# Optimization experiments

Measured on AMD Instinct MI355X. Metric: run time of the kernel, lower is better.

Reference implementation:

```python
import jax, jax.numpy as jnp
import numpy as np

EPS = 1e-8
INTRA_MARGIN_USED = 1.5  # combine() swaps margins: intra gets delta_dist
INTER_MARGIN_USED = 0.5  # inter gets delta_var
INTRA_W, INTER_W, REG_W = 1.0, 1.0, 0.001


def setup_inputs() -> dict:
    key = jax.random.key(0)
    k1, k2 = jax.random.split(key)
    N, D, K = 1000000, 32, 64
    features = jax.random.normal(k1, (N, D), dtype=jnp.float32)
    labels = jax.random.randint(k2, (N,), 0, K, dtype=jnp.int64 if jax.config.jax_enable_x64 else jnp.int32)
    return {"features": features, "labels": labels, "num_clusters": K}


def reference(features, labels, num_clusters):
    K = int(num_clusters)
    N, D = features.shape
    ones = jnp.ones((N,), dtype=features.dtype)
    counts = jax.ops.segment_sum(ones, labels, num_segments=K)            # (K,)
    sums = jax.ops.segment_sum(features, labels, num_segments=K)          # (K, D)
    safe_counts = jnp.maximum(counts, 1.0)
    means = sums / safe_counts[:, None]                                   # (K, D) cluster centroids

    # --- intra (variance) loss; margin = 1.5 due to original swap ---
    diff = features - means[labels] + EPS                                 # (N, D)
    dists = jnp.sqrt(jnp.sum(diff * diff, axis=1))                        # (N,)
    hinge2 = jnp.square(jnp.maximum(dists - INTRA_MARGIN_USED, 0.0))
    per_cluster = jax.ops.segment_sum(hinge2, labels, num_segments=K) / safe_counts
    intra_loss = jnp.mean(per_cluster)

    # --- inter (distance) loss; margin = 0.5 due to original swap ---
    pdiff = means[:, None, :] - means[None, :, :] + EPS                   # (K, K, D)
    pdist = jnp.sqrt(jnp.sum(pdiff * pdiff, axis=-1))                     # (K, K)
    hinge = jnp.square(jnp.maximum(2.0 * INTER_MARGIN_USED - pdist, 0.0))
    offdiag = 1.0 - jnp.eye(K, dtype=features.dtype)
    inter_loss = jnp.sum(hinge * offdiag) / float((K - 1) * K)

    # --- regularization ---
    reg_loss = jnp.mean(jnp.sqrt(jnp.sum(jnp.square(means + EPS), axis=1)))

    total = INTRA_W * intra_loss + INTER_W * inter_loss + REG_W * reg_loss
    return total
```

## Files before the change

### kernel.cpp

```cpp
#include <hip/hip_runtime.h>
#include <math.h>


#define EPS_F 1e-8f
constexpr int D = 32;
constexpr int K = 64;
constexpr int NPTS = 1024;
constexpr int P1 = K * D + K;
constexpr int NCH = 64;
constexpr int NBLK2 = 2048;
constexpr int MPAD = 40;

__global__ __launch_bounds__(256, 4) void pass1_kernel(
    const float* __restrict__ feat, const int* __restrict__ lab,
    float* __restrict__ part1, float* __restrict__ sums, int N)
{
    __shared__ int            s_lab[NPTS];
    __shared__ unsigned short s_idx[NPTS];
    __shared__ int            s_hist[K];
    __shared__ int            s_pref[K];
    __shared__ int            s_cur[K];

    const int tid = threadIdx.x;
    const long long base = (long long)blockIdx.x * NPTS;
    int npts = (int)((long long)N - base);
    if (npts > NPTS) npts = NPTS;

    if (blockIdx.x == 0)
        for (int e = tid; e < P1; e += 256) sums[e] = 0.f;

    if (tid < K) s_hist[tid] = 0;
    __syncthreads();

    const int n4 = npts >> 2;
    for (int i4 = tid; i4 < n4; i4 += 256) {
        const int4 v = ((const int4*)(lab + base))[i4];
        s_lab[i4 * 4 + 0] = v.x; s_lab[i4 * 4 + 1] = v.y;
        s_lab[i4 * 4 + 2] = v.z; s_lab[i4 * 4 + 3] = v.w;
        atomicAdd(&s_hist[v.x], 1); atomicAdd(&s_hist[v.y], 1);
        atomicAdd(&s_hist[v.z], 1); atomicAdd(&s_hist[v.w], 1);
    }
    for (int i = (n4 << 2) + tid; i < npts; i += 256) {
        const int l = lab[base + i];
        s_lab[i] = l;
        atomicAdd(&s_hist[l], 1);
    }
    __syncthreads();

    if (tid < 64) {
        const int h = s_hist[tid];
        int v = h;
        for (int off = 1; off < 64; off <<= 1) {
            const int up = __shfl_up(v, off);
            if (tid >= off) v += up;
        }
        s_pref[tid] = v - h;
        s_cur[tid]  = v - h;
    }
    __syncthreads();

    for (int i = tid; i < npts; i += 256) {
        const int l = s_lab[i];
        const int pos = atomicAdd(&s_cur[l], 1);
        s_idx[pos] = (unsigned short)i;
    }
    __syncthreads();

    const int k = tid >> 2, q = tid & 3;
    const int start = s_pref[k], len = s_hist[k];
    float4 a0 = {0.f, 0.f, 0.f, 0.f}, a1 = {0.f, 0.f, 0.f, 0.f};
    int i = 0;
    for (; i + 4 <= len; i += 4) {
        const int i0 = s_idx[start + i + 0];
        const int i1 = s_idx[start + i + 1];
        const int i2 = s_idx[start + i + 2];
        const int i3 = s_idx[start + i + 3];
        const float4* r0 = (const float4*)(feat + (base + i0) * D + q * 8);
        const float4* r1 = (const float4*)(feat + (base + i1) * D + q * 8);
        const float4* r2 = (const float4*)(feat + (base + i2) * D + q * 8);
        const float4* r3 = (const float4*)(feat + (base + i3) * D + q * 8);
        const float4 x0 = r0[0], y0 = r0[1];
        const float4 x1 = r1[0], y1 = r1[1];
        const float4 x2 = r2[0], y2 = r2[1];
        const float4 x3 = r3[0], y3 = r3[1];
        a0.x += (x0.x + x1.x) + (x2.x + x3.x);
        a0.y += (x0.y + x1.y) + (x2.y + x3.y);
        a0.z += (x0.z + x1.z) + (x2.z + x3.z);
        a0.w += (x0.w + x1.w) + (x2.w + x3.w);
        a1.x += (y0.x + y1.x) + (y2.x + y3.x);
        a1.y += (y0.y + y1.y) + (y2.y + y3.y);
        a1.z += (y0.z + y1.z) + (y2.z + y3.z);
        a1.w += (y0.w + y1.w) + (y2.w + y3.w);
    }
    for (; i < len; ++i) {
        const int i0 = s_idx[start + i];
        const float4* r0 = (const float4*)(feat + (base + i0) * D + q * 8);
        const float4 x0 = r0[0], y0 = r0[1];
        a0.x += x0.x; a0.y += x0.y; a0.z += x0.z; a0.w += x0.w;
        a1.x += y0.x; a1.y += y0.y; a1.z += y0.z; a1.w += y0.w;
    }
    float* outp = part1 + (long long)blockIdx.x * P1;
    ((float4*)outp)[tid * 2 + 0] = a0;
    ((float4*)outp)[tid * 2 + 1] = a1;
    if (tid < K) outp[K * D + tid] = (float)s_hist[tid];
}

__global__ __launch_bounds__(256) void reduce1_kernel(
    const float* __restrict__ part1, float* __restrict__ sums,
    int chsz, int nblk1)
{
    const int e = blockIdx.x * 256 + threadIdx.x;
    if (e >= P1) return;
    const int y = blockIdx.y;
    const int b0 = y * chsz;
    int b1 = b0 + chsz; if (b1 > nblk1) b1 = nblk1;
    float s = 0.f;
    for (int b = b0; b < b1; b++) s += part1[(long long)b * P1 + e];
    atomicAdd(&sums[e], s);
}

__global__ __launch_bounds__(256, 4) void pass2_kernel(
    const float* __restrict__ feat, const int* __restrict__ lab,
    const float* __restrict__ sums,
    float* __restrict__ hpart, float* __restrict__ ir, int N)
{
    __shared__ float s_m[K * MPAD];
    __shared__ float s_ic[K];
    __shared__ float s_red[256];
    const int tid = threadIdx.x;

    for (int e = tid; e < K * D; e += 256) {
        const float c = sums[K * D + (e >> 5)];
        s_m[(e >> 5) * MPAD + (e & 31)] = sums[e] / fmaxf(c, 1.0f);
    }
    if (tid < K) s_ic[tid] = 1.0f / fmaxf(sums[K * D + tid], 1.0f);
    __syncthreads();

    float racc = 0.f;
    const long long stride = (long long)NBLK2 * 256;
    for (long long p = (long long)blockIdx.x * 256 + tid; p < N; p += stride) {
        const int l = lab[p];
        const float4* frow = (const float4*)(feat + p * D);
        float4 fv[8];
        #pragma unroll
        for (int j = 0; j < 8; j++) fv[j] = frow[j];
        const float* mrow = s_m + l * MPAD;
        float d2 = 0.f;
        #pragma unroll
        for (int j = 0; j < 8; j++) {
            const float4 mv = *(const float4*)(mrow + j * 4);
            const float dx = fv[j].x - mv.x + EPS_F;
            const float dy = fv[j].y - mv.y + EPS_F;
            const float dz = fv[j].z - mv.z + EPS_F;
            const float dw = fv[j].w - mv.w + EPS_F;
            d2 += dx * dx + dy * dy + dz * dz + dw * dw;
        }
        const float h = fmaxf(sqrtf(d2) - 1.5f, 0.f);
        racc += h * h * s_ic[l];
    }
    s_red[tid] = racc;
    __syncthreads();
    for (int st = 128; st; st >>= 1) { if (tid < st) s_red[tid] += s_red[tid + st]; __syncthreads(); }
    if (tid == 0) hpart[blockIdx.x] = s_red[0];

    if (blockIdx.x != 0) return;
    __syncthreads();
    float mj[32];
    const int j = tid & 63;
    #pragma unroll
    for (int d = 0; d < 32; d++) mj[d] = s_m[j * MPAD + d];
    float isum = 0.f;
    const int igrp = tid >> 6;
    for (int ii = 0; ii < 16; ii++) {
        const int i = igrp * 16 + ii;
        const float4* srow = (const float4*)(s_m + i * MPAD);
        float d2 = 0.f;
        #pragma unroll
        for (int q = 0; q < 8; q++) {
            const float4 mv = srow[q];
            const float b0 = mv.x - mj[q * 4 + 0] + EPS_F;
            const float b1 = mv.y - mj[q * 4 + 1] + EPS_F;
            const float b2 = mv.z - mj[q * 4 + 2] + EPS_F;
            const float b3 = mv.w - mj[q * 4 + 3] + EPS_F;
            d2 += b0 * b0 + b1 * b1 + b2 * b2 + b3 * b3;
        }
        if (i != j) {
            const float h = fmaxf(1.0f - sqrtf(d2), 0.f);
            isum += h * h;
        }
    }
    s_red[tid] = isum;
    __syncthreads();
    for (int st = 128; st; st >>= 1) { if (tid < st) s_red[tid] += s_red[tid + st]; __syncthreads(); }
    if (tid == 0) ir[0] = s_red[0] * (1.0f / ((K - 1) * K));
    __syncthreads();

    float r = 0.f;
    if (tid < 64) {
        float d2 = 0.f;
        #pragma unroll
        for (int d = 0; d < 32; d++) { const float t = mj[d] + EPS_F; d2 += t * t; }
        r = sqrtf(d2);
    }
    s_red[tid] = r;
    __syncthreads();
    for (int st = 128; st; st >>= 1) { if (tid < st) s_red[tid] += s_red[tid + st]; __syncthreads(); }
    if (tid == 0) ir[1] = s_red[0] * (1.0f / K);
}

__global__ __launch_bounds__(256) void final_kernel(
    const float* __restrict__ hpart, const float* __restrict__ ir,
    float* __restrict__ out)
{
    __shared__ float s_red[256];
    const int tid = threadIdx.x;
    float hs = 0.f;
    for (int b = tid; b < NBLK2; b += 256) hs += hpart[b];
    s_red[tid] = hs;
    __syncthreads();
    for (int st = 128; st; st >>= 1) { if (tid < st) s_red[tid] += s_red[tid + st]; __syncthreads(); }
    if (tid == 0) out[0] = s_red[0] * (1.0f / K) + ir[0] + 0.001f * ir[1];
}

extern "C" void kernel_launch(void* const* d_in, const int* in_sizes, int n_in,
                              void* d_out, int out_size, void* d_ws, size_t ws_size,
                              hipStream_t stream)
{
    const float* feat = (const float*)d_in[0];
    const int*   lab  = (const int*)d_in[1];
    const int N = in_sizes[1];

    float* ws = (float*)d_ws;

    const int nblk1 = (N + NPTS - 1) / NPTS;
    const int chsz  = (nblk1 + NCH - 1) / NCH;

    float* sums  = ws;
    float* ir    = sums + P1;
    float* hpart = ir + 4;
    float* part1 = hpart + NBLK2;

    pass1_kernel<<<nblk1, 256, 0, stream>>>(feat, lab, part1, sums, N);
    reduce1_kernel<<<dim3((P1 + 255) / 256, NCH), 256, 0, stream>>>(part1, sums, chsz, nblk1);
    pass2_kernel<<<NBLK2, 256, 0, stream>>>(feat, lab, sums, hpart, ir, N);
    final_kernel<<<1, 256, 0, stream>>>(hpart, ir, (float*)d_out);
}
```

Baseline: 61.99 us.

## Stage feature tiles in LDS for coalesced per-cluster sums in pass1

The first pass now loads each block's feature tile with contiguous float4 loads into a padded shared-memory tile. The per-cluster gather-and-sum then reads from LDS instead of issuing scattered global loads by sorted index. Labels are read one per thread, the tile shrinks to 512 points, and blocks grow to 512 threads, each thread summing one float4 column slice per cluster. The aim is to replace uncoalesced global gathers with coalesced streaming. The cost is large LDS use per block, which limits occupancy, and twice as many partial rows for the reduction kernel to read.

```diff
diff --git a/kernel.cpp b/kernel.cpp
--- a/kernel.cpp
+++ b/kernel.cpp
@@ -5,46 +5,52 @@
 #define EPS_F 1e-8f
 constexpr int D = 32;
 constexpr int K = 64;
-constexpr int NPTS = 1024;
+constexpr int NPTS = 512;
+constexpr int RSTRIDE = 36;
 constexpr int P1 = K * D + K;
 constexpr int NCH = 64;
 constexpr int NBLK2 = 2048;
 constexpr int MPAD = 40;
 
-__global__ __launch_bounds__(256, 4) void pass1_kernel(
+constexpr int L_TILE = NPTS * RSTRIDE;
+constexpr int L_IDX  = L_TILE;
+constexpr int L_HIST = L_IDX + NPTS / 2;
+constexpr int L_PREF = L_HIST + K;
+constexpr int L_CUR  = L_PREF + K;
+constexpr int L_TOTAL = L_CUR + K;
+
+__global__ __launch_bounds__(512) void pass1_kernel(
     const float* __restrict__ feat, const int* __restrict__ lab,
     float* __restrict__ part1, float* __restrict__ sums, int N)
 {
-    __shared__ int            s_lab[NPTS];
-    __shared__ unsigned short s_idx[NPTS];
-    __shared__ int            s_hist[K];
-    __shared__ int            s_pref[K];
-    __shared__ int            s_cur[K];
+    extern __shared__ float smem[];
+    float*          s_tile = smem;
+    unsigned short* s_idx  = (unsigned short*)(smem + L_IDX);
+    int*            s_hist = (int*)(smem + L_HIST);
+    int*            s_pref = (int*)(smem + L_PREF);
+    int*            s_cur  = (int*)(smem + L_CUR);
 
     const int tid = threadIdx.x;
     const long long base = (long long)blockIdx.x * NPTS;
     int npts = (int)((long long)N - base);
     if (npts > NPTS) npts = NPTS;
+    const int nf4 = npts * 8;
 
     if (blockIdx.x == 0)
-        for (int e = tid; e < P1; e += 256) sums[e] = 0.f;
+        for (int e = tid; e < P1; e += 512) sums[e] = 0.f;
+
+    const int myl = (tid < npts) ? lab[base + tid] : -1;
+    float4 st[8];
+    const float4* fsrc = (const float4*)(feat + base * D);
+    #pragma unroll
+    for (int u = 0; u < 8; u++) {
+        const int g = tid + u * 512;
+        if (g < nf4) st[u] = fsrc[g];
+    }
 
     if (tid < K) s_hist[tid] = 0;
     __syncthreads();
-
-    const int n4 = npts >> 2;
-    for (int i4 = tid; i4 < n4; i4 += 256) {
-        const int4 v = ((const int4*)(lab + base))[i4];
-        s_lab[i4 * 4 + 0] = v.x; s_lab[i4 * 4 + 1] = v.y;
-        s_lab[i4 * 4 + 2] = v.z; s_lab[i4 * 4 + 3] = v.w;
-        atomicAdd(&s_hist[v.x], 1); atomicAdd(&s_hist[v.y], 1);
-        atomicAdd(&s_hist[v.z], 1); atomicAdd(&s_hist[v.w], 1);
-    }
-    for (int i = (n4 << 2) + tid; i < npts; i += 256) {
-        const int l = lab[base + i];
-        s_lab[i] = l;
-        atomicAdd(&s_hist[l], 1);
-    }
+    if (myl >= 0) atomicAdd(&s_hist[myl], 1);
     __syncthreads();
 
     if (tid < 64) {
@@ -59,49 +65,44 @@
     }
     __syncthreads();
 
-    for (int i = tid; i < npts; i += 256) {
-        const int l = s_lab[i];
-        const int pos = atomicAdd(&s_cur[l], 1);
-        s_idx[pos] = (unsigned short)i;
-    }
-    __syncthreads();
-
-    const int k = tid >> 2, q = tid & 3;
+    if (myl >= 0) {
+        const int pos = atomicAdd(&s_cur[myl], 1);
+        s_idx[pos] = (unsigned short)tid;
+    }
+
+    #pragma unroll
+    for (int u = 0; u < 8; u++) {
+        const int g = tid + u * 512;
+        if (g < nf4)
+            *(float4*)&s_tile[(g >> 3) * RSTRIDE + (g & 7) * 4] = st[u];
+    }
+    __syncthreads();
+
+    const int k = tid >> 3, sub = tid & 7;
     const int start = s_pref[k], len = s_hist[k];
-    float4 a0 = {0.f, 0.f, 0.f, 0.f}, a1 = {0.f, 0.f, 0.f, 0.f};
+    float4 a = {0.f, 0.f, 0.f, 0.f};
     int i = 0;
     for (; i + 4 <= len; i += 4) {
         const int i0 = s_idx[start + i + 0];
         const int i1 = s_idx[start + i + 1];
         const int i2 = s_idx[start + i + 2];
         const int i3 = s_idx[start + i + 3];
-        const float4* r0 = (const float4*)(feat + (base + i0) * D + q * 8);
-        const float4* r1 = (const float4*)(feat + (base + i1) * D + q * 8);
-        const float4* r2 = (const float4*)(feat + (base + i2) * D + q * 8);
-        const float4* r3 = (const float4*)(feat + (base + i3) * D + q * 8);
-        const float4 x0 = r0[0], y0 = r0[1];
-        const float4 x1 = r1[0], y1 = r1[1];
-        const float4 x2 = r2[0], y2 = r2[1];
-        const float4 x3 = r3[0], y3 = r3[1];
-        a0.x += (x0.x + x1.x) + (x2.x + x3.x);
-        a0.y += (x0.y + x1.y) + (x2.y + x3.y);
-        a0.z += (x0.z + x1.z) + (x2.z + x3.z);
-        a0.w += (x0.w + x1.w) + (x2.w + x3.w);
-        a1.x += (y0.x + y1.x) + (y2.x + y3.x);
-        a1.y += (y0.y + y1.y) + (y2.y + y3.y);
-        a1.z += (y0.z + y1.z) + (y2.z + y3.z);
-        a1.w += (y0.w + y1.w) + (y2.w + y3.w);
+        const float4 x0 = *(const float4*)&s_tile[i0 * RSTRIDE + sub * 4];
+        const float4 x1 = *(const float4*)&s_tile[i1 * RSTRIDE + sub * 4];
+        const float4 x2 = *(const float4*)&s_tile[i2 * RSTRIDE + sub * 4];
+        const float4 x3 = *(const float4*)&s_tile[i3 * RSTRIDE + sub * 4];
+        a.x += (x0.x + x1.x) + (x2.x + x3.x);
+        a.y += (x0.y + x1.y) + (x2.y + x3.y);
+        a.z += (x0.z + x1.z) + (x2.z + x3.z);
+        a.w += (x0.w + x1.w) + (x2.w + x3.w);
     }
     for (; i < len; ++i) {
         const int i0 = s_idx[start + i];
-        const float4* r0 = (const float4*)(feat + (base + i0) * D + q * 8);
-        const float4 x0 = r0[0], y0 = r0[1];
-        a0.x += x0.x; a0.y += x0.y; a0.z += x0.z; a0.w += x0.w;
-        a1.x += y0.x; a1.y += y0.y; a1.z += y0.z; a1.w += y0.w;
+        const float4 x0 = *(const float4*)&s_tile[i0 * RSTRIDE + sub * 4];
+        a.x += x0.x; a.y += x0.y; a.z += x0.z; a.w += x0.w;
     }
     float* outp = part1 + (long long)blockIdx.x * P1;
-    ((float4*)outp)[tid * 2 + 0] = a0;
-    ((float4*)outp)[tid * 2 + 1] = a1;
+    ((float4*)outp)[tid] = a;
     if (tid < K) outp[K * D + tid] = (float)s_hist[tid];
 }
 
@@ -240,7 +241,7 @@
     float* hpart = ir + 4;
     float* part1 = hpart + NBLK2;
 
-    pass1_kernel<<<nblk1, 256, 0, stream>>>(feat, lab, part1, sums, N);
+    pass1_kernel<<<nblk1, 512, L_TOTAL * 4, stream>>>(feat, lab, part1, sums, N);
     reduce1_kernel<<<dim3((P1 + 255) / 256, NCH), 256, 0, stream>>>(part1, sums, chsz, nblk1);
     pass2_kernel<<<NBLK2, 256, 0, stream>>>(feat, lab, sums, hpart, ir, N);
     final_kernel<<<1, 256, 0, stream>>>(hpart, ir, (float*)d_out);
```

Result: slower. 105.6 us (+70.3%).
